# Kernel tuning notes

Hardware: AMD Instinct MI355X
Metric: run time of the kernel (lower is better)

The kernel has to match this reference:

```python
import jax, jax.numpy as jnp
import numpy as np

N_REACHES = 4096
N_STEPS = 96
DT = 3600.0  # routing timestep (s), default from MuskingumCungeRouter


def safe_pow(base, exp, eps=1e-6):
    # AD-safe power: exp(e * log(max(b, eps)))
    return jnp.exp(exp * jnp.log(jnp.maximum(base, eps)))


def setup_inputs() -> dict:
    key = jax.random.key(0)
    ks = jax.random.split(key, 10)
    n, T = N_REACHES, N_STEPS
    u = lambda k, lo, hi, shape: jax.random.uniform(k, shape, minval=lo, maxval=hi)
    lateral_inflows = u(ks[0], 0.0, 5.0, (T, n))          # m^3/s lateral inflow
    initial_Q = u(ks[1], 0.1, 10.0, (n,))
    lengths = u(ks[2], 500.0, 10000.0, (n,))              # reach length (m)
    slopes = u(ks[3], 1e-4, 0.05, (n,))                   # bed slope
    manning_n = u(ks[4], 0.02, 0.08, (n,))
    width_coef = u(ks[5], 2.0, 10.0, (n,))
    width_exp = u(ks[6], 0.4, 0.6, (n,))                  # ~0.5 typical
    depth_coef = u(ks[7], 0.2, 0.6, (n,))
    depth_exp = u(ks[8], 0.25, 0.35, (n,))                # ~0.3 typical
    # Strictly lower-triangular sparse adjacency: reach i receives from j < i
    # (valid topological order), ~4 upstream links per reach on average.
    upstream_mask = jnp.tril(jax.random.uniform(ks[9], (n, n)) < (4.0 / n), k=-1)
    is_outlet = jnp.arange(n) == n - 1
    return dict(lateral_inflows=lateral_inflows, initial_Q=initial_Q,
                lengths=lengths, slopes=slopes, manning_n=manning_n,
                width_coef=width_coef, width_exp=width_exp,
                depth_coef=depth_coef, depth_exp=depth_exp,
                upstream_mask=upstream_mask, is_outlet=is_outlet)


def _mc_coeffs(Q, L, S, mn, wc, we, dc, de, dt):
    """Vectorized Muskingum-Cunge coefficients for all reaches.

    Faithful fusion of compute_channel_geometry -> compute_velocity_manning ->
    compute_celerity -> compute_muskingum_params. Q here is Q_ref = max(state.Q, 0.1),
    which only depends on the previous state, so hoisting out of the per-reach
    scan is mathematically identical to the original.
    """
    Qs = jnp.maximum(Q, 0.01)
    W = wc * safe_pow(Qs, we)
    D = dc * safe_pow(Qs, de)
    A = W * D
    R = A / (W + 2.0 * D)                      # hydraulic radius
    safe_S = jnp.maximum(S, 1e-6)
    V = (1.0 / jnp.maximum(mn, 1e-3)) * safe_pow(R, 2.0 / 3.0) * jnp.sqrt(safe_S)
    c = jnp.maximum((5.0 / 3.0) * V, 0.01)     # kinematic wave celerity
    K = jnp.maximum(L / c, dt * 0.1)
    X = jnp.clip(0.5 * (1.0 - Q / (W * c * safe_S * L + 1e-6)), 0.0, 0.5)
    den = 2.0 * K * (1.0 - X) + dt
    C0 = jnp.maximum((dt - 2.0 * K * X) / den, 0.0)
    C1 = jnp.maximum((dt + 2.0 * K * X) / den, 0.0)
    C2 = jnp.maximum((2.0 * K * (1.0 - X) - dt) / den, 0.0)
    tot = C0 + C1 + C2
    return C0 / tot, C1 / tot, C2 / tot


def _route(lateral_inflows, initial_Q, lengths, slopes, manning_n,
           width_coef, width_exp, depth_coef, depth_exp,
           upstream_mask, is_outlet, dt=DT):
    n = lengths.shape[0]

    def step(state, lateral):
        Q, Q_prev, I_prev = state
        Q_ref = jnp.maximum(Q, 0.1)
        C0, C1, C2 = _mc_coeffs(Q_ref, lengths, slopes, manning_n,
                                width_coef, width_exp, depth_coef, depth_exp, dt)

        # Sequential topological sweep: masked reduction over already-routed reaches.
        def process(Q_acc, i):
            upstream_Q = jnp.sum(jnp.where(upstream_mask[i], Q_acc, 0.0))
            I_curr = upstream_Q + lateral[i]
            Q_out = jnp.maximum(C0[i] * I_curr + C1[i] * I_prev[i] + C2[i] * Q_prev[i], 0.0)
            return Q_acc.at[i].set(Q_out), I_curr

        Q_final, I_all = jax.lax.scan(process, jnp.zeros(n, lateral.dtype), jnp.arange(n))
        outlet_Q = jnp.sum(jnp.where(is_outlet, Q_final, 0.0))
        return (Q_final, Q, I_all), outlet_Q

    init = (initial_Q, initial_Q, jnp.zeros(n, initial_Q.dtype))
    _, outlet_series = jax.lax.scan(step, init, lateral_inflows)
    return outlet_series  # [n_timesteps]


def reference(lateral_inflows, initial_Q, lengths, slopes, manning_n,
              width_coef, width_exp, depth_coef, depth_exp,
              upstream_mask, is_outlet):
    return _route(lateral_inflows, initial_Q, lengths, slopes, manning_n,
                  width_coef, width_exp, depth_coef, depth_exp,
                  upstream_mask, is_outlet)
```

## Files before the change

kernel.cpp:

```cpp
#include <hip/hip_runtime.h>

#define NR 4096
#define NT 96
#define NNZ_CAP 10240
#define SREM_CAP 4096
#define LONG_CAP 4096
#define WLDS 8
#define SSTR 4112
#define DHIST 32
#define DTSTEP 3600.0f
#define LOG2_1E6 -19.931568f

__device__ __forceinline__ float RCP(float x) { return __builtin_amdgcn_rcpf(x); }
__device__ __forceinline__ float EXP2(float x) { return __builtin_amdgcn_exp2f(x); }
__device__ __forceinline__ float LOG2(float x) { return __builtin_amdgcn_logf(x); }

__global__ void mc_build(const int* __restrict__ mask, int* __restrict__ rowBase,
                         int* __restrict__ rowCnt, int* __restrict__ gctr,
                         unsigned short* __restrict__ cols) {
  __shared__ unsigned short tmp[80];
  __shared__ int baseS;
  int row = blockIdx.x;
  int lane = threadIdx.x;
  const int* rs = mask + (size_t)row * NR;
  int total = 0;
  for (int j0 = 0; j0 < NR; j0 += 64) {
    int j = j0 + lane;
    int pred = (rs[j] != 0);
    unsigned long long m = __ballot(pred);
    if (pred) {
      int pos = total + __popcll(m & ((1ull << lane) - 1ull));
      if (pos < 80) tmp[pos] = (unsigned short)j;
    }
    total += __popcll(m);
  }
  if (total > 80) total = 80;
  if (lane == 0) {
    int b = atomicAdd(gctr, total);
    rowBase[row] = b;
    rowCnt[row] = total;
    baseS = b;
  }
  __syncthreads();
  int base = baseS;
  for (int e = lane; e < total; e += 64) {
    int p = base + e;
    if (p < NNZ_CAP) cols[p] = tmp[e];
  }
}

__global__ __launch_bounds__(1024) void mc_prep(
    const int* __restrict__ rowBase, const int* __restrict__ rowCnt,
    const int* __restrict__ gctr, const unsigned short* __restrict__ colsOld,
    unsigned short* __restrict__ orderG, unsigned short* __restrict__ levNG,
    unsigned short* __restrict__ scolG, unsigned int* __restrict__ sremMeta,
    unsigned int* __restrict__ longMeta, unsigned short* __restrict__ sremG,
    unsigned short* __restrict__ longG, unsigned char* __restrict__ lsG,
    int* __restrict__ meta) {
  __shared__ unsigned short cols_s[NNZ_CAP];
  __shared__ unsigned char lev_s[NR];
  __shared__ unsigned short newid_s[NR];
  __shared__ unsigned short order_s[NR];
  __shared__ unsigned char lsrc_s[NR];
  __shared__ int cnt[1024];
  __shared__ int sbuf[1024];
  __shared__ int maxLevS, flagS;
  const int tid = threadIdx.x;
  int nnz = gctr[0];
  if (nnz > NNZ_CAP) nnz = NNZ_CAP;
  for (int e = tid; e < nnz; e += 1024) cols_s[e] = colsOld[e];

  int b_r[4], e_r[4];
#pragma unroll
  for (int k = 0; k < 4; ++k) {
    int i = 4 * tid + k;
    int b = rowBase[i];
    if (b > NNZ_CAP) b = NNZ_CAP;
    int e = b + rowCnt[i];
    if (e > NNZ_CAP) e = NNZ_CAP;
    b_r[k] = b;
    e_r[k] = e;
    lev_s[i] = 0;
    lsrc_s[i] = 0;
  }
  if (tid == 0) maxLevS = 0;
  __syncthreads();

  for (int pass = 0; pass < 48; ++pass) {
    if (tid == 0) flagS = 0;
    __syncthreads();
    int ch = 0;
#pragma unroll
    for (int k = 0; k < 4; ++k) {
      int i = 4 * tid + k;
      int lv = 0;
      for (int e = b_r[k]; e < e_r[k]; ++e) {
        int l2 = (int)lev_s[cols_s[e]] + 1;
        lv = lv > l2 ? lv : l2;
      }
      if (lv > 127) lv = 127;
      if (lv > (int)lev_s[i]) {
        lev_s[i] = (unsigned char)lv;
        ch = 1;
      }
    }
    if (ch) flagS = 1;
    __syncthreads();
    int done = (flagS == 0);
    __syncthreads();
    if (done) break;
  }
  int lm = 0;
#pragma unroll
  for (int k = 0; k < 4; ++k) {
    int l = lev_s[4 * tid + k];
    lm = lm > l ? lm : l;
  }
  atomicMax(&maxLevS, lm);
  __syncthreads();
  const int maxLev = maxLevS;
  if (tid == 0) {
    meta[0] = maxLev + 1;
    meta[2] = (maxLev >= DHIST) ? 1 : 0;
  }
  if (maxLev >= DHIST) {
#pragma unroll
    for (int k = 0; k < 4; ++k) {
      int i = 4 * tid + k;
      orderG[i] = (unsigned short)i;
      levNG[i] = (unsigned short)lev_s[i];
    }
    return;
  }

  cnt[tid] = 0;
  __syncthreads();
  int bkt_r[4];
#pragma unroll
  for (int k = 0; k < 4; ++k) {
    int i = 4 * tid + k;
    int d = e_r[k] - b_r[k];
    if (d > 31) d = 31;
    int bkt = ((int)lev_s[i]) * 32 + d;
    bkt_r[k] = bkt;
    atomicAdd(&cnt[bkt], 1);
  }
  __syncthreads();
  int v = cnt[tid];
  sbuf[tid] = v;
  __syncthreads();
  for (int off = 1; off < 1024; off <<= 1) {
    int add = tid >= off ? sbuf[tid - off] : 0;
    __syncthreads();
    sbuf[tid] += add;
    __syncthreads();
  }
  cnt[tid] = sbuf[tid] - v;
  __syncthreads();
#pragma unroll
  for (int k = 0; k < 4; ++k) {
    int i = 4 * tid + k;
    int pos = atomicAdd(&cnt[bkt_r[k]], 1);
    order_s[pos] = (unsigned short)i;
    newid_s[i] = (unsigned short)pos;
  }
  __syncthreads();

#pragma unroll
  for (int k = 0; k < 4; ++k) {
    int p = 4 * tid + k;
    int oldi = order_s[p];
    orderG[p] = (unsigned short)oldi;
    int lp = (int)lev_s[oldi];
    levNG[p] = (unsigned short)lp;
    int b = rowBase[oldi];
    if (b > NNZ_CAP) b = NNZ_CAP;
    int e = b + rowCnt[oldi];
    if (e > NNZ_CAP) e = NNZ_CAP;
    int nS = 0, nR = 0, nL = 0;
    for (int ee = b; ee < e; ++ee) {
      int lag = lp - (int)lev_s[cols_s[ee]];
      if (lag < WLDS) {
        if (nS < 4) ++nS; else ++nR;
      } else ++nL;
    }
    if (nR > 63) nR = 63;
    if (nL > 63) nL = 63;
    int sB = nR ? atomicAdd(&meta[4], nR) : 0;
    int lB = nL ? atomicAdd(&meta[5], nL) : 0;
    if (sB > SREM_CAP) sB = SREM_CAP;
    if (sB + nR > SREM_CAP) nR = SREM_CAP - sB;
    if (lB > LONG_CAP) lB = LONG_CAP;
    if (lB + nL > LONG_CAP) nL = LONG_CAP - lB;
    unsigned short sc[4] = {4096, 4096, 4096, 4096};
    int iS = 0, cR = 0, cL = 0;
    for (int ee = b; ee < e; ++ee) {
      int cOld = cols_s[ee];
      int cN = newid_s[cOld];
      int lag = lp - (int)lev_s[cOld];
      if (lag < WLDS) {
        if (iS < 4) sc[iS++] = (unsigned short)cN;
        else if (cR < nR) { sremG[sB + cR] = (unsigned short)cN; ++cR; }
      } else {
        if (cL < nL) { longG[lB + cL] = (unsigned short)cN; ++cL; }
        lsrc_s[cN] = 1;
      }
    }
    scolG[4 * p + 0] = sc[0];
    scolG[4 * p + 1] = sc[1];
    scolG[4 * p + 2] = sc[2];
    scolG[4 * p + 3] = sc[3];
    sremMeta[p] = (unsigned)sB | ((unsigned)nR << 20);
    longMeta[p] = (unsigned)lB | ((unsigned)nL << 20);
  }
  if (tid == 0) meta[1] = newid_s[NR - 1];
  __syncthreads();
#pragma unroll
  for (int k = 0; k < 4; ++k) {
    int p = 4 * tid + k;
    lsG[p] = lsrc_s[p];
  }
}

__global__ void mc_permlat(const float* __restrict__ lat,
                           const unsigned short* __restrict__ orderG,
                           float* __restrict__ latP) {
  int g = blockIdx.x * 256 + threadIdx.x;
  int t = g >> 12, p = g & 4095;
  latP[g] = lat[t * NR + orderG[p]];
}

__global__ __launch_bounds__(1024, 4) void mc_route(
    const float* __restrict__ lat, const float* __restrict__ latP,
    const float* __restrict__ initQ, const float* __restrict__ Lg,
    const float* __restrict__ Sg, const float* __restrict__ mng,
    const float* __restrict__ wcg, const float* __restrict__ weg,
    const float* __restrict__ dcg, const float* __restrict__ deg,
    const int* __restrict__ rowBase, const int* __restrict__ rowCnt,
    const unsigned short* __restrict__ colsOld,
    const unsigned short* __restrict__ orderG,
    const unsigned short* __restrict__ levNG,
    const unsigned short* __restrict__ scolG,
    const unsigned int* __restrict__ sremMeta,
    const unsigned int* __restrict__ longMeta,
    const unsigned short* __restrict__ sremG,
    const unsigned short* __restrict__ longG,
    const unsigned char* __restrict__ lsG, const int* __restrict__ meta,
    float* Qhist, float* __restrict__ out, int usePerm) {
  __shared__ float win_s[WLDS * SSTR];
  __shared__ unsigned short srem_s[SREM_CAP];
  __shared__ unsigned short long_s[LONG_CAP];
  const int tid = threadIdx.x;
  const int nlv = meta[0];
  const int fb = meta[2];
  const int outletNew = meta[1];
  const float* latB = usePerm ? latP : lat;

  if (!fb) {
    int sc_r[4][4];
    int lev_r[4], io_r[4], ls_r[4], wOff_r[4];
    unsigned int smeta_r[4], lmeta_r[4];
    const float* latp_r[4];
    float lwc_r[4], we_r[4], ldc_r[4], de_r[4], lvk_r[4], SL_r[4], L_r[4];
    float ip_r[4], q1_r[4], q2_r[4], latN_r[4];

    int nSrem = meta[4];
    if (nSrem > SREM_CAP) nSrem = SREM_CAP;
    int nLong = meta[5];
    if (nLong > LONG_CAP) nLong = LONG_CAP;
    for (int e = tid; e < nSrem; e += 1024) srem_s[e] = sremG[e];
    for (int e = tid; e < nLong; e += 1024) long_s[e] = longG[e];
    if (tid < WLDS) win_s[tid * SSTR + 4096] = 0.f;

#pragma unroll
    for (int k = 0; k < 4; ++k) {
      int p = tid + k * 1024;
      int oldi = orderG[p];
      lev_r[k] = (int)levNG[p];
      uint2 cc = *(const uint2*)(scolG + 4 * p);
      sc_r[k][0] = cc.x & 0xFFFFu;
      sc_r[k][1] = cc.x >> 16;
      sc_r[k][2] = cc.y & 0xFFFFu;
      sc_r[k][3] = cc.y >> 16;
      smeta_r[k] = sremMeta[p];
      lmeta_r[k] = longMeta[p];
      ls_r[k] = (int)lsG[p];
      io_r[k] = (p == outletNew);
      float Lv = Lg[oldi];
      float sS = fmaxf(Sg[oldi], 1e-6f);
      float mnv = fmaxf(mng[oldi], 1e-3f);
      lvk_r[k] = 0.7369656f + 0.5f * LOG2(sS) - LOG2(mnv);
      SL_r[k] = sS * Lv;
      L_r[k] = Lv;
      lwc_r[k] = LOG2(wcg[oldi]);
      we_r[k] = weg[oldi];
      ldc_r[k] = LOG2(dcg[oldi]);
      de_r[k] = deg[oldi];
      float q0 = initQ[oldi];
      q1_r[k] = q0;
      q2_r[k] = q0;
      ip_r[k] = 0.f;
      wOff_r[k] = 0;
      latp_r[k] = latB + (usePerm ? p : oldi);
      latN_r[k] = *latp_r[k];
    }
    __syncthreads();

#define BODY(k, tt)                                                             \
  {                                                                             \
    const int p = tid + (k)*1024;                                               \
    const float latv = latN_r[k];                                               \
    float Qref = fmaxf(q1_r[k], 0.1f);                                          \
    float lq = LOG2(Qref);                                                      \
    float lgW = fmaf(we_r[k], lq, lwc_r[k]);                                    \
    float W = EXP2(lgW);                                                        \
    float aD = fmaf(de_r[k], lq, ldc_r[k]);                                     \
    float Dd = EXP2(aD);                                                        \
    float lgR = fmaxf(lgW + aD - LOG2(fmaf(2.f, Dd, W)), LOG2_1E6);             \
    float c = fmaxf(EXP2(fmaf(0.66666667f, lgR, lvk_r[k])), 0.01f);             \
    float K = fmaxf(L_r[k] * RCP(c), 360.f);                                    \
    float X = fmaxf(0.5f - 0.5f * Qref * RCP(fmaf(W * c, SL_r[k], 1e-6f)), 0.f);\
    float twoKX = 2.f * K * X;                                                  \
    float C0 = fmaxf(DTSTEP - twoKX, 0.f);                                      \
    float C1 = DTSTEP + twoKX;                                                  \
    float C2 = fmaxf(2.f * K - twoKX - DTSTEP, 0.f);                            \
    float inv = RCP(C0 + C1 + C2);                                              \
    const int wB = wOff_r[k];                                                   \
    float v0 = win_s[wB + sc_r[k][0]];                                          \
    float v1 = win_s[wB + sc_r[k][1]];                                          \
    float v2 = win_s[wB + sc_r[k][2]];                                          \
    float v3 = win_s[wB + sc_r[k][3]];                                          \
    float sup = (v0 + v1) + (v2 + v3);                                          \
    const int sC = (int)(smeta_r[k] >> 20);                                     \
    if (sC) {                                                                   \
      const int sB = (int)(smeta_r[k] & 0xFFFFFu);                              \
      for (int e = 0; e < sC; ++e) sup += win_s[wB + srem_s[sB + e]];           \
    }                                                                           \
    const int lC = (int)(lmeta_r[k] >> 20);                                     \
    if (lC) {                                                                   \
      const int lB = (int)(lmeta_r[k] & 0xFFFFFu);                              \
      const float* qb = Qhist + (((tt)&31) << 12);                              \
      for (int e = 0; e < lC; ++e) sup += qb[long_s[lB + e]];                   \
    }                                                                           \
    float Icurr = sup + latv;                                                   \
    float Qout = fmaxf((C0 * Icurr + C1 * ip_r[k] + C2 * q2_r[k]) * inv, 0.f);  \
    win_s[wB + p] = Qout;                                                       \
    if (ls_r[k]) Qhist[(((tt)&31) << 12) | p] = Qout;                           \
    if (io_r[k]) out[tt] = Qout;                                                \
    ip_r[k] = Icurr;                                                            \
    q2_r[k] = q1_r[k];                                                          \
    q1_r[k] = Qout;                                                             \
    wOff_r[k] = (wOff_r[k] == (WLDS - 1) * SSTR) ? 0 : wOff_r[k] + SSTR;        \
    latp_r[k] += ((tt) + 1 < NT) ? NR : 0;                                      \
    latN_r[k] = *latp_r[k];                                                     \
  }

#define BODYC(k, s)                                                            \
  {                                                                            \
    int t = (s)-lev_r[k];                                                      \
    if ((unsigned)t < (unsigned)NT) BODY(k, t)                                 \
  }

    for (int s = 0; s < nlv - 1; ++s) {
#pragma unroll
      for (int k = 0; k < 4; ++k) BODYC(k, s);
      __syncthreads();
    }
    for (int s = nlv - 1; s < NT; ++s) {
#pragma unroll
      for (int k = 0; k < 4; ++k) {
        int t = s - lev_r[k];
        BODY(k, t);
      }
      __syncthreads();
    }
    for (int s = NT; s < NT + nlv - 1; ++s) {
#pragma unroll
      for (int k = 0; k < 4; ++k) BODYC(k, s);
      __syncthreads();
    }
  } else {
    unsigned short* colsF = (unsigned short*)win_s;
    int b_r[4], e_r[4], lev_r[4];
    float lwc_r[4], we_r[4], ldc_r[4], de_r[4], lvk_r[4], SL_r[4], L_r[4];
    float ip_r[4], q1_r[4], q2_r[4];
    for (int e = tid; e < NNZ_CAP; e += 1024) colsF[e] = colsOld[e];
#pragma unroll
    for (int k = 0; k < 4; ++k) {
      int i = tid + k * 1024;
      lev_r[k] = (int)levNG[i];
      int b = rowBase[i];
      if (b > NNZ_CAP) b = NNZ_CAP;
      int e = b + rowCnt[i];
      if (e > NNZ_CAP) e = NNZ_CAP;
      b_r[k] = b;
      e_r[k] = e;
      float Lv = Lg[i];
      float sS = fmaxf(Sg[i], 1e-6f);
      float mnv = fmaxf(mng[i], 1e-3f);
      lvk_r[k] = 0.7369656f + 0.5f * LOG2(sS) - LOG2(mnv);
      SL_r[k] = sS * Lv;
      L_r[k] = Lv;
      lwc_r[k] = LOG2(wcg[i]);
      we_r[k] = weg[i];
      ldc_r[k] = LOG2(dcg[i]);
      de_r[k] = deg[i];
      float q0 = initQ[i];
      q1_r[k] = q0;
      q2_r[k] = q0;
      ip_r[k] = 0.f;
    }
    __syncthreads();
    for (int t = 0; t < NT; ++t) {
      for (int l = 0; l < nlv; ++l) {
#pragma unroll
        for (int k = 0; k < 4; ++k) {
          if (lev_r[k] == l) {
            int i = tid + k * 1024;
            float latv = lat[t * NR + i];
            float Qref = fmaxf(q1_r[k], 0.1f);
            float lq = LOG2(Qref);
            float lgW = fmaf(we_r[k], lq, lwc_r[k]);
            float W = EXP2(lgW);
            float aD = fmaf(de_r[k], lq, ldc_r[k]);
            float Dd = EXP2(aD);
            float lgR = fmaxf(lgW + aD - LOG2(fmaf(2.f, Dd, W)), LOG2_1E6);
            float c = fmaxf(EXP2(fmaf(0.66666667f, lgR, lvk_r[k])), 0.01f);
            float K = fmaxf(L_r[k] * RCP(c), 360.f);
            float X =
                fmaxf(0.5f - 0.5f * Qref * RCP(fmaf(W * c, SL_r[k], 1e-6f)), 0.f);
            float twoKX = 2.f * K * X;
            float C0 = fmaxf(DTSTEP - twoKX, 0.f);
            float C1 = DTSTEP + twoKX;
            float C2 = fmaxf(2.f * K - twoKX - DTSTEP, 0.f);
            float inv = RCP(C0 + C1 + C2);
            float sup = 0.f;
            for (int e = b_r[k]; e < e_r[k]; ++e) sup += Qhist[colsF[e]];
            float Icurr = sup + latv;
            float Qout =
                fmaxf((C0 * Icurr + C1 * ip_r[k] + C2 * q2_r[k]) * inv, 0.f);
            Qhist[i] = Qout;
            ip_r[k] = Icurr;
            q2_r[k] = q1_r[k];
            q1_r[k] = Qout;
            if (i == NR - 1) out[t] = Qout;
          }
        }
        __syncthreads();
      }
    }
  }
}

extern "C" void kernel_launch(void* const* d_in, const int* in_sizes, int n_in,
                              void* d_out, int out_size, void* d_ws, size_t ws_size,
                              hipStream_t stream) {
  const float* lat = (const float*)d_in[0];
  const float* iQ = (const float*)d_in[1];
  const float* Lg = (const float*)d_in[2];
  const float* Sg = (const float*)d_in[3];
  const float* mng = (const float*)d_in[4];
  const float* wcg = (const float*)d_in[5];
  const float* weg = (const float*)d_in[6];
  const float* dcg = (const float*)d_in[7];
  const float* deg = (const float*)d_in[8];
  const int* mask = (const int*)d_in[9];
  float* out = (float*)d_out;

  char* w = (char*)d_ws;
  int* rowBase = (int*)w;                        w += NR * 4;
  int* rowCnt = (int*)w;                         w += NR * 4;
  int* gctr = (int*)w;                           w += 16;
  int* meta = (int*)w;                           w += 32;
  unsigned short* colsOld = (unsigned short*)w;  w += NNZ_CAP * 2;
  unsigned short* orderG = (unsigned short*)w;   w += NR * 2;
  unsigned short* levNG = (unsigned short*)w;    w += NR * 2;
  unsigned short* scolG = (unsigned short*)w;    w += NR * 4 * 2;
  unsigned int* sremMeta = (unsigned int*)w;     w += NR * 4;
  unsigned int* longMeta = (unsigned int*)w;     w += NR * 4;
  unsigned short* sremG = (unsigned short*)w;    w += SREM_CAP * 2;
  unsigned short* longG = (unsigned short*)w;    w += LONG_CAP * 2;
  unsigned char* lsG = (unsigned char*)w;        w += NR;
  w += 16 - ((size_t)w & 15);
  float* Qhist = (float*)w;                      w += (size_t)DHIST * NR * 4;
  float* latP = (float*)w;                       w += (size_t)NT * NR * 4;
  size_t need = (size_t)(w - (char*)d_ws);
  int usePerm = (ws_size >= need) ? 1 : 0;

  hipMemsetAsync(gctr, 0, 48, stream);
  mc_build<<<NR, 64, 0, stream>>>(mask, rowBase, rowCnt, gctr, colsOld);
  mc_prep<<<1, 1024, 0, stream>>>(rowBase, rowCnt, gctr, colsOld, orderG, levNG,
                                  scolG, sremMeta, longMeta, sremG, longG, lsG,
                                  meta);
  if (usePerm)
    mc_permlat<<<(NT * NR) / 256, 256, 0, stream>>>(lat, orderG, latP);
  mc_route<<<1, 1024, 0, stream>>>(lat, latP, iQ, Lg, Sg, mng, wcg, weg, dcg,
                                   deg, rowBase, rowCnt, colsOld, orderG, levNG,
                                   scolG, sremMeta, longMeta, sremG, longG, lsG,
                                   meta, Qhist, out, usePerm);
}
```

Before: 521.3 us.

## Use custom partial-waitcnt barrier, early loads, and log-domain coefficient math

Replaces __syncthreads in the wavefront loop with a barrier that waits only for LDS operations and leaves up to six global loads outstanding, so next-step lateral prefetches can stay in flight across the barrier. The lateral prefetch and the upstream gathers now run at the start of each body, and the third and fourth short-column reads are skipped when a reach has two or fewer near upstream links (the count is packed into the metadata). The Muskingum X and K terms are computed in log2 space, which removes reciprocals. The barrier relies on a hand-counted vmcnt; if that count is wrong, Qhist reads could race with writes.

```diff
diff --git a/kernel.cpp b/kernel.cpp
--- a/kernel.cpp
+++ b/kernel.cpp
@@ -14,6 +14,12 @@
 __device__ __forceinline__ float RCP(float x) { return __builtin_amdgcn_rcpf(x); }
 __device__ __forceinline__ float EXP2(float x) { return __builtin_amdgcn_exp2f(x); }
 __device__ __forceinline__ float LOG2(float x) { return __builtin_amdgcn_logf(x); }
+
+__device__ __forceinline__ void phase_barrier() {
+  asm volatile("s_waitcnt lgkmcnt(0) vmcnt(6)" ::: "memory");
+  __builtin_amdgcn_s_barrier();
+  asm volatile("" ::: "memory");
+}
 
 __global__ void mc_build(const int* __restrict__ mask, int* __restrict__ rowBase,
                          int* __restrict__ rowCnt, int* __restrict__ gctr,
@@ -210,7 +216,7 @@
     scolG[4 * p + 1] = sc[1];
     scolG[4 * p + 2] = sc[2];
     scolG[4 * p + 3] = sc[3];
-    sremMeta[p] = (unsigned)sB | ((unsigned)nR << 20);
+    sremMeta[p] = (unsigned)sB | ((unsigned)nR << 20) | ((unsigned)iS << 26);
     longMeta[p] = (unsigned)lB | ((unsigned)nL << 20);
   }
   if (tid == 0) meta[1] = newid_s[NR - 1];
@@ -258,10 +264,10 @@
 
   if (!fb) {
     int sc_r[4][4];
-    int lev_r[4], io_r[4], ls_r[4], wOff_r[4];
+    int lev_r[4], io_r[4], ls_r[4], wOff_r[4], nsc_r[4];
     unsigned int smeta_r[4], lmeta_r[4];
     const float* latp_r[4];
-    float lwc_r[4], we_r[4], ldc_r[4], de_r[4], lvk_r[4], SL_r[4], L_r[4];
+    float lwc_r[4], we_r[4], ldc_r[4], de_r[4], lvk_r[4], lgSL_r[4], L_r[4];
     float ip_r[4], q1_r[4], q2_r[4], latN_r[4];
 
     int nSrem = meta[4];
@@ -283,6 +289,7 @@
       sc_r[k][2] = cc.y & 0xFFFFu;
       sc_r[k][3] = cc.y >> 16;
       smeta_r[k] = sremMeta[p];
+      nsc_r[k] = (int)(smeta_r[k] >> 26);
       lmeta_r[k] = longMeta[p];
       ls_r[k] = (int)lsG[p];
       io_r[k] = (p == outletNew);
@@ -290,7 +297,7 @@
       float sS = fmaxf(Sg[oldi], 1e-6f);
       float mnv = fmaxf(mng[oldi], 1e-3f);
       lvk_r[k] = 0.7369656f + 0.5f * LOG2(sS) - LOG2(mnv);
-      SL_r[k] = sS * Lv;
+      lgSL_r[k] = LOG2(sS * Lv);
       L_r[k] = Lv;
       lwc_r[k] = LOG2(wcg[oldi]);
       we_r[k] = weg[oldi];
@@ -310,6 +317,27 @@
   {                                                                             \
     const int p = tid + (k)*1024;                                               \
     const float latv = latN_r[k];                                               \
+    latp_r[k] += ((tt) + 1 < NT) ? NR : 0;                                      \
+    latN_r[k] = *latp_r[k];              \
+    const int wB = wOff_r[k];                                                   \
+    float v0 = win_s[wB + sc_r[k][0]];                                          \
+    float v1 = win_s[wB + sc_r[k][1]];                                          \
+    float v23 = 0.f;                                                            \
+    if (nsc_r[k] > 2)                                                           \
+      v23 = win_s[wB + sc_r[k][2]] + win_s[wB + sc_r[k][3]];                    \
+    float ssum = 0.f;                                                           \
+    const int sC = (int)((smeta_r[k] >> 20) & 63);                              \
+    if (sC) {                                                                   \
+      const int sB = (int)(smeta_r[k] & 0xFFFFFu);                              \
+      for (int e = 0; e < sC; ++e) ssum += win_s[wB + srem_s[sB + e]];          \
+    }                                                                           \
+    float lsum = 0.f;                                                           \
+    const int lC = (int)(lmeta_r[k] >> 20);                                     \
+    if (lC) {                                                                   \
+      const int lB = (int)(lmeta_r[k] & 0xFFFFFu);                              \
+      const float* qb = Qhist + (((tt)&31) << 12);                              \
+      for (int e = 0; e < lC; ++e) lsum += qb[long_s[lB + e]];                  \
+    }                                                                           \
     float Qref = fmaxf(q1_r[k], 0.1f);                                          \
     float lq = LOG2(Qref);                                                      \
     float lgW = fmaf(we_r[k], lq, lwc_r[k]);                                    \
@@ -317,31 +345,17 @@
     float aD = fmaf(de_r[k], lq, ldc_r[k]);                                     \
     float Dd = EXP2(aD);                                                        \
     float lgR = fmaxf(lgW + aD - LOG2(fmaf(2.f, Dd, W)), LOG2_1E6);             \
-    float c = fmaxf(EXP2(fmaf(0.66666667f, lgR, lvk_r[k])), 0.01f);             \
-    float K = fmaxf(L_r[k] * RCP(c), 360.f);                                    \
-    float X = fmaxf(0.5f - 0.5f * Qref * RCP(fmaf(W * c, SL_r[k], 1e-6f)), 0.f);\
-    float twoKX = 2.f * K * X;                                                  \
+    float lgc = fmaf(0.66666667f, lgR, lvk_r[k]);                               \
+    float K = fmaxf(L_r[k] * EXP2(-lgc), 360.f);                                \
+    float ratio = EXP2(lq - lgW - lgc - lgSL_r[k]);                             \
+    float X = fmaxf(fmaf(-0.5f, ratio, 0.5f), 0.f);                             \
+    float twoK = K + K;                                                         \
+    float twoKX = twoK * X;                                                     \
     float C0 = fmaxf(DTSTEP - twoKX, 0.f);                                      \
     float C1 = DTSTEP + twoKX;                                                  \
-    float C2 = fmaxf(2.f * K - twoKX - DTSTEP, 0.f);                            \
+    float C2 = fmaxf(twoK - twoKX - DTSTEP, 0.f);                               \
     float inv = RCP(C0 + C1 + C2);                                              \
-    const int wB = wOff_r[k];                                                   \
-    float v0 = win_s[wB + sc_r[k][0]];                                          \
-    float v1 = win_s[wB + sc_r[k][1]];                                          \
-    float v2 = win_s[wB + sc_r[k][2]];                                          \
-    float v3 = win_s[wB + sc_r[k][3]];                                          \
-    float sup = (v0 + v1) + (v2 + v3);                                          \
-    const int sC = (int)(smeta_r[k] >> 20);                                     \
-    if (sC) {                                                                   \
-      const int sB = (int)(smeta_r[k] & 0xFFFFFu);                              \
-      for (int e = 0; e < sC; ++e) sup += win_s[wB + srem_s[sB + e]];           \
-    }                                                                           \
-    const int lC = (int)(lmeta_r[k] >> 20);                                     \
-    if (lC) {                                                                   \
-      const int lB = (int)(lmeta_r[k] & 0xFFFFFu);                              \
-      const float* qb = Qhist + (((tt)&31) << 12);                              \
-      for (int e = 0; e < lC; ++e) sup += qb[long_s[lB + e]];                   \
-    }                                                                           \
+    float sup = ((v0 + v1) + v23) + (ssum + lsum);                              \
     float Icurr = sup + latv;                                                   \
     float Qout = fmaxf((C0 * Icurr + C1 * ip_r[k] + C2 * q2_r[k]) * inv, 0.f);  \
     win_s[wB + p] = Qout;                                                       \
@@ -351,8 +365,6 @@
     q2_r[k] = q1_r[k];                                                          \
     q1_r[k] = Qout;                                                             \
     wOff_r[k] = (wOff_r[k] == (WLDS - 1) * SSTR) ? 0 : wOff_r[k] + SSTR;        \
-    latp_r[k] += ((tt) + 1 < NT) ? NR : 0;                                      \
-    latN_r[k] = *latp_r[k];                                                     \
   }
 
 #define BODYC(k, s)                                                            \
@@ -364,7 +376,7 @@
     for (int s = 0; s < nlv - 1; ++s) {
 #pragma unroll
       for (int k = 0; k < 4; ++k) BODYC(k, s);
-      __syncthreads();
+      phase_barrier();
     }
     for (int s = nlv - 1; s < NT; ++s) {
 #pragma unroll
@@ -372,12 +384,12 @@
         int t = s - lev_r[k];
         BODY(k, t);
       }
-      __syncthreads();
+      phase_barrier();
     }
     for (int s = NT; s < NT + nlv - 1; ++s) {
 #pragma unroll
       for (int k = 0; k < 4; ++k) BODYC(k, s);
-      __syncthreads();
+      phase_barrier();
     }
   } else {
     unsigned short* colsF = (unsigned short*)win_s;
```

New measurement: 465.1 us, median of 2. 10.8% less time.
